# Performance work log

Measured on AMD Instinct MI355X. Metric: run time of the kernel, lower is better.

The kernel has to match this reference:

```python
import jax, jax.numpy as jnp
import numpy as np

B, N_IN, N_OUT, H = 64, 5023, 5023, 256
EPS = 1e-12  # matches torch F.normalize default eps


def setup_inputs() -> dict:
    key = jax.random.key(0)
    k1, k2, k3, k4 = jax.random.split(key, 4)
    return {
        "x": jax.random.normal(k1, (B, N_IN, 3), dtype=jnp.float32),
        "key_w": jax.random.normal(k2, (N_IN, H), dtype=jnp.float32) * (1.0 / np.sqrt(H)),
        "query_w": jax.random.normal(k3, (H, N_OUT), dtype=jnp.float32) * (1.0 / np.sqrt(H)),
        "value_w": jax.random.normal(k4, (3, 3), dtype=jnp.float32),
    }


def reference(x, key_w, query_w, value_w):
    # v = nn.Linear(3,3,bias=False)(x): x @ W^T        [B, N_in, 3]
    v = jnp.einsum("bnd,ed->bne", x, value_w)
    # score = (key @ query) / sqrt(hidden_dim)          [N_in, N_out]
    scale = jnp.asarray(key_w.shape[-1], x.dtype) ** 0.5
    score = jnp.matmul(key_w, query_w) / scale
    # L1 normalization along dim=1 (F.normalize p=1)
    l1 = jnp.sum(jnp.abs(score), axis=1, keepdims=True)
    score = score / jnp.maximum(l1, EPS)
    # y = score.T @ v (dropout is identity in eval / p=0) [B, N_out, 3]
    return jnp.einsum("io,bid->bod", score, v)
```

## Files before the change

kernel.cpp:

```cpp
#include <hip/hip_runtime.h>
#include <hip/hip_bf16.h>

#define N_IN   5023
#define B_SZ   64
#define H_DIM  256
#define NPAD   5120
#define NBD    192
#define SPLITZ 20
#define OUT_ELEMS (B_SZ * N_IN * 3)

typedef short bf16x8 __attribute__((ext_vector_type(8)));
typedef float f32x4  __attribute__((ext_vector_type(4)));

__device__ inline void async_copy16(const void* g, void* l) {
    __builtin_amdgcn_global_load_lds(
        (const __attribute__((address_space(1))) unsigned int*)g,
        (__attribute__((address_space(3))) unsigned int*)l,
        16, 0, 0);
}

__global__ void conv_key_all(const float* __restrict__ kw, short* __restrict__ keyb,
                             short* __restrict__ keyT, float* __restrict__ l1) {
    __shared__ float tile[32][33];
    const int hb = blockIdx.x * 32;
    const int ib = blockIdx.y * 32;
    const int tx = threadIdx.x;
    const int ty = threadIdx.y;
    __hip_bfloat16* kb = (__hip_bfloat16*)keyb;
    __hip_bfloat16* kt = (__hip_bfloat16*)keyT;
    for (int j = 0; j < 32; j += 8) {
        int i = ib + ty + j;
        int h = hb + tx;
        float v = (i < N_IN) ? kw[(size_t)i * H_DIM + h] : 0.0f;
        tile[ty + j][tx] = v;
        kb[(size_t)i * H_DIM + h] = __float2bfloat16(v);
    }
    __syncthreads();
    for (int j = 0; j < 32; j += 8) {
        int h = hb + ty + j;
        int i = ib + tx;
        kt[(size_t)h * NPAD + i] = __float2bfloat16(tile[tx][ty + j]);
    }
    if (blockIdx.x == 0 && ty == 0) l1[ib + tx] = 0.0f;
}

__global__ void conv_qt(const float* __restrict__ qw, short* __restrict__ qtb) {
    __shared__ float tile[32][33];
    const int hb = blockIdx.x * 32;
    const int ob = blockIdx.y * 32;
    const int tx = threadIdx.x;
    const int ty = threadIdx.y;
    for (int j = 0; j < 32; j += 8) {
        int h = hb + ty + j;
        int o = ob + tx;
        tile[ty + j][tx] = (o < N_IN) ? qw[(size_t)h * N_IN + o] * 0.0625f : 0.0f;
    }
    __syncthreads();
    __hip_bfloat16* qt = (__hip_bfloat16*)qtb;
    for (int j = 0; j < 32; j += 8) {
        int o = ob + ty + j;
        int h = hb + tx;
        qt[(size_t)o * H_DIM + h] = __float2bfloat16(tile[tx][ty + j]);
    }
}

__launch_bounds__(256)
__global__ void gemm_l1(const short* __restrict__ qt, const short* __restrict__ keyb,
                        float* __restrict__ l1) {
    __shared__ short As[128 * 64];
    __shared__ short Bs[128 * 64];
    const int bm = blockIdx.x, bn = blockIdx.y;
    const int tid = threadIdx.x, lane = tid & 63, wid = tid >> 6;
    const int wave_m = wid >> 1, wave_n = wid & 1;
    const int srow = lane >> 3;
    const int scol = (lane & 7) * 8;

    f32x4 acc[4][4];
    const f32x4 zf = {0.f, 0.f, 0.f, 0.f};
    for (int a = 0; a < 4; ++a)
        for (int b = 0; b < 4; ++b) acc[a][b] = zf;

    for (int kb = 0; kb < H_DIM; kb += 64) {
        __syncthreads();
        for (int c = 0; c < 4; ++c) {
            int q = wid * 4 + c;
            int row = q * 8 + srow;
            async_copy16(qt   + (size_t)(bm * 128 + row) * H_DIM + kb + scol, As + q * 512);
            async_copy16(keyb + (size_t)(bn * 128 + row) * H_DIM + kb + scol, Bs + q * 512);
        }
        __syncthreads();
        for (int kk = 0; kk < 64; kk += 32) {
            bf16x8 af[4], bf[4];
            int ko = kk + (lane >> 4) * 8;
            for (int t = 0; t < 4; ++t) {
                af[t] = *(const bf16x8*)(As + (wave_m * 64 + t * 16 + (lane & 15)) * 64 + ko);
                bf[t] = *(const bf16x8*)(Bs + (wave_n * 64 + t * 16 + (lane & 15)) * 64 + ko);
            }
            for (int tm = 0; tm < 4; ++tm)
                for (int tn = 0; tn < 4; ++tn)
                    acc[tm][tn] = __builtin_amdgcn_mfma_f32_16x16x32_bf16(
                        af[tm], bf[tn], acc[tm][tn], 0, 0, 0);
        }
    }

    const int quad = lane >> 4, cit = lane & 15;
    for (int tn = 0; tn < 4; ++tn) {
        int ig = bn * 128 + wave_n * 64 + tn * 16 + cit;
        float p = 0.0f;
        for (int tm = 0; tm < 4; ++tm) {
            f32x4 c = acc[tm][tn];
            p += fabsf(c.x) + fabsf(c.y) + fabsf(c.z) + fabsf(c.w);
        }
        p += __shfl_xor(p, 16);
        p += __shfl_xor(p, 32);
        if (quad == 0) atomicAdd(&l1[ig], p);
    }
}

__global__ void build_vmat(const float* __restrict__ x, const float* __restrict__ vw,
                           const float* __restrict__ l1, short* __restrict__ vmatT) {
    int idx = blockIdx.x * 256 + threadIdx.x;
    if (idx >= B_SZ * NPAD) return;
    int b = idx / NPAD, i = idx % NPAD;
    __hip_bfloat16* vt = (__hip_bfloat16*)vmatT;
    if (i < N_IN) {
        const float* xp = x + ((size_t)b * N_IN + i) * 3;
        float x0 = xp[0], x1 = xp[1], x2 = xp[2];
        float r = 1.0f / fmaxf(l1[i], 1e-12f);
        for (int e = 0; e < 3; ++e) {
            float v = x0 * vw[e * 3 + 0] + x1 * vw[e * 3 + 1] + x2 * vw[e * 3 + 2];
            vt[(size_t)(b * 3 + e) * NPAD + i] = __float2bfloat16(v * r);
        }
    } else {
        for (int e = 0; e < 3; ++e)
            vt[(size_t)(b * 3 + e) * NPAD + i] = __float2bfloat16(0.0f);
    }
}

__launch_bounds__(256)
__global__ void gemm3(const short* __restrict__ vmatT, const short* __restrict__ keyT,
                      float* __restrict__ part2) {
    __shared__ short As[192 * 64];
    __shared__ short Bs[64 * 64];
    const int bh = blockIdx.x;
    const int z  = blockIdx.y;
    const int tid = threadIdx.x, lane = tid & 63, wid = tid >> 6;
    const int wave_m = wid >> 1, wave_n = wid & 1;
    const int srow = lane >> 3, scol = (lane & 7) * 8;
    const int quad = lane >> 4, cit = lane & 15;

    f32x4 acc[6][2];
    const f32x4 zf = {0.f, 0.f, 0.f, 0.f};
    for (int a = 0; a < 6; ++a)
        for (int b = 0; b < 2; ++b) acc[a][b] = zf;

    const int kbeg = z * (NPAD / SPLITZ);
    for (int kb = kbeg; kb < kbeg + NPAD / SPLITZ; kb += 64) {
        __syncthreads();
        for (int c = 0; c < 6; ++c) {
            int q = wid * 6 + c;
            int row = q * 8 + srow;
            async_copy16(vmatT + (size_t)row * NPAD + kb + scol, As + q * 512);
        }
        for (int c = 0; c < 2; ++c) {
            int q = wid * 2 + c;
            int row = q * 8 + srow;
            async_copy16(keyT + (size_t)(bh * 64 + row) * NPAD + kb + scol, Bs + q * 512);
        }
        __syncthreads();
        for (int kk = 0; kk < 64; kk += 32) {
            bf16x8 af[6], bf[2];
            int ko = kk + quad * 8;
            for (int t = 0; t < 6; ++t)
                af[t] = *(const bf16x8*)(As + (wave_m * 96 + t * 16 + cit) * 64 + ko);
            for (int t = 0; t < 2; ++t)
                bf[t] = *(const bf16x8*)(Bs + (wave_n * 32 + t * 16 + cit) * 64 + ko);
            for (int tm = 0; tm < 6; ++tm)
                for (int tn = 0; tn < 2; ++tn)
                    acc[tm][tn] = __builtin_amdgcn_mfma_f32_16x16x32_bf16(
                        af[tm], bf[tn], acc[tm][tn], 0, 0, 0);
        }
    }

    float* pz = part2 + (size_t)z * (NBD * H_DIM);
    for (int tn = 0; tn < 2; ++tn) {
        int h = bh * 64 + wave_n * 32 + tn * 16 + cit;
        for (int tm = 0; tm < 6; ++tm) {
            int bd0 = wave_m * 96 + tm * 16 + quad * 4;
            f32x4 c = acc[tm][tn];
            for (int r = 0; r < 4; ++r)
                pz[(size_t)(bd0 + r) * H_DIM + h] = c[r];
        }
    }
}

__global__ void reduce_T(const float* __restrict__ part2, short* __restrict__ T) {
    int idx = blockIdx.x * 256 + threadIdx.x;
    float s = 0.0f;
    for (int z = 0; z < SPLITZ; ++z)
        s += part2[(size_t)z * (NBD * H_DIM) + idx];
    ((__hip_bfloat16*)T)[idx] = __float2bfloat16(s);
}

#define CS_PITCH 196
__launch_bounds__(256)
__global__ void gemm4(const short* __restrict__ qt, const short* __restrict__ T,
                      float* __restrict__ out) {
    __shared__ char smem[64 * CS_PITCH * 4];
    short* As = (short*)smem;
    short* Bs = As + 64 * 64;
    const int bm = blockIdx.x;
    const int tid = threadIdx.x, lane = tid & 63, wid = tid >> 6;
    const int wave_m = wid >> 1, wave_n = wid & 1;
    const int srow = lane >> 3, scol = (lane & 7) * 8;
    const int quad = lane >> 4, cit = lane & 15;

    f32x4 acc[2][6];
    const f32x4 zf = {0.f, 0.f, 0.f, 0.f};
    for (int a = 0; a < 2; ++a)
        for (int b = 0; b < 6; ++b) acc[a][b] = zf;

    for (int kb = 0; kb < H_DIM; kb += 64) {
        __syncthreads();
        for (int c = 0; c < 2; ++c) {
            int q = wid * 2 + c;
            int row = q * 8 + srow;
            async_copy16(qt + (size_t)(bm * 64 + row) * H_DIM + kb + scol, As + q * 512);
        }
        for (int c = 0; c < 6; ++c) {
            int q = wid * 6 + c;
            int row = q * 8 + srow;
            async_copy16(T + (size_t)row * H_DIM + kb + scol, Bs + q * 512);
        }
        __syncthreads();
        for (int kk = 0; kk < 64; kk += 32) {
            bf16x8 af[2], bf[6];
            int ko = kk + quad * 8;
            for (int t = 0; t < 2; ++t)
                af[t] = *(const bf16x8*)(As + (wave_m * 32 + t * 16 + cit) * 64 + ko);
            for (int t = 0; t < 6; ++t)
                bf[t] = *(const bf16x8*)(Bs + (wave_n * 96 + t * 16 + cit) * 64 + ko);
            for (int tm = 0; tm < 2; ++tm)
                for (int tn = 0; tn < 6; ++tn)
                    acc[tm][tn] = __builtin_amdgcn_mfma_f32_16x16x32_bf16(
                        af[tm], bf[tn], acc[tm][tn], 0, 0, 0);
        }
    }

    __syncthreads();
    float* cs = (float*)smem;
    for (int tn = 0; tn < 6; ++tn) {
        int bd = wave_n * 96 + tn * 16 + cit;
        for (int tm = 0; tm < 2; ++tm) {
            int o0 = wave_m * 32 + tm * 16 + quad * 4;
            f32x4 c = acc[tm][tn];
            for (int r = 0; r < 4; ++r)
                cs[(o0 + r) * CS_PITCH + bd] = c[r];
        }
    }
    __syncthreads();
    for (int it = 0; it < 48; ++it) {
        int flat = it * 256 + tid;
        int b = flat / NBD;
        int w = flat - b * NBD;
        int o_l = w / 3, d = w - o_l * 3;
        int og = bm * 64 + o_l;
        if (og < N_IN)
            out[(size_t)b * (N_IN * 3) + (size_t)og * 3 + d] =
                cs[o_l * CS_PITCH + b * 3 + d];
    }
}

extern "C" void kernel_launch(void* const* d_in, const int* in_sizes, int n_in,
                              void* d_out, int out_size, void* d_ws, size_t ws_size,
                              hipStream_t stream) {
    const float* x  = (const float*)d_in[0];
    const float* kw = (const float*)d_in[1];
    const float* qw = (const float*)d_in[2];
    const float* vw = (const float*)d_in[3];
    float* out = (float*)d_out;

    char* w = (char*)d_ws;
    short* keyb  = (short*)(w + 0);
    short* qtb   = (short*)(w + 2621440);
    short* keyT  = (short*)(w + 5242880);
    short* vmatT = (short*)(w + 7864320);
    float* l1    = (float*)(w + 9830400);
    float* part2 = (float*)(w + 9850880);
    short* T     = (short*)(w + 13783040);

    conv_key_all<<<dim3(H_DIM / 32, NPAD / 32), dim3(32, 8), 0, stream>>>(kw, keyb, keyT, l1);
    conv_qt<<<dim3(H_DIM / 32, NPAD / 32), dim3(32, 8), 0, stream>>>(qw, qtb);
    gemm_l1<<<dim3(NPAD / 128, NPAD / 128), 256, 0, stream>>>(qtb, keyb, l1);
    build_vmat<<<(B_SZ * NPAD) / 256, 256, 0, stream>>>(x, vw, l1, vmatT);
    gemm3<<<dim3(H_DIM / 64, SPLITZ), 256, 0, stream>>>(vmatT, keyT, part2);
    reduce_T<<<(NBD * H_DIM) / 256, 256, 0, stream>>>(part2, T);
    gemm4<<<NPAD / 64, 256, 0, stream>>>(qtb, T, out);
}
```

Before: 115.1 us.

## Compute L1 norm GEMM in FP8 with swizzled LDS layout

Adds a conversion kernel that packs the bf16 query and key matrices into FP8, with the query scaled by 16 to keep values in FP8 range. The L1-norm GEMM then uses the fp8 MFMA instruction over 128-wide K chunks with an XOR-swizzled LDS layout, halving the operand bytes and the number of K iterations. build_vmat divides the 16x scale back out. The trade is an extra conversion pass over both matrices and lower precision in the row-sum norms.

```diff
diff --git a/kernel.cpp b/kernel.cpp
--- a/kernel.cpp
+++ b/kernel.cpp
@@ -64,46 +64,67 @@
     }
 }
 
+#define HALF_ELEMS (NPAD * H_DIM / 2)
+__global__ void conv_fp8(const short* __restrict__ qtb, const short* __restrict__ keyb,
+                         unsigned short* __restrict__ q8, unsigned short* __restrict__ k8) {
+    int idx = blockIdx.x * 256 + threadIdx.x;
+    bool isK = idx >= HALF_ELEMS;
+    int p = isK ? idx - HALF_ELEMS : idx;
+    const __hip_bfloat16* src = (const __hip_bfloat16*)(isK ? keyb : qtb);
+    float a = __bfloat162float(src[2 * p]);
+    float b = __bfloat162float(src[2 * p + 1]);
+    if (!isK) { a *= 16.0f; b *= 16.0f; }
+    int packed = __builtin_amdgcn_cvt_pk_fp8_f32(a, b, 0, false);
+    (isK ? k8 : q8)[p] = (unsigned short)(packed & 0xFFFF);
+}
+
 __launch_bounds__(256)
-__global__ void gemm_l1(const short* __restrict__ qt, const short* __restrict__ keyb,
+__global__ void gemm_l1(const unsigned char* __restrict__ q8,
+                        const unsigned char* __restrict__ k8,
                         float* __restrict__ l1) {
-    __shared__ short As[128 * 64];
-    __shared__ short Bs[128 * 64];
+    __shared__ unsigned char As8[128 * 128];
+    __shared__ unsigned char Bs8[128 * 128];
     const int bm = blockIdx.x, bn = blockIdx.y;
     const int tid = threadIdx.x, lane = tid & 63, wid = tid >> 6;
     const int wave_m = wid >> 1, wave_n = wid & 1;
-    const int srow = lane >> 3;
-    const int scol = (lane & 7) * 8;
+    const int r = lane >> 3;
+    const int s = lane & 7;
+    const int quad = lane >> 4, cit = lane & 15;
+    const int xk = cit & 7;
 
     f32x4 acc[4][4];
     const f32x4 zf = {0.f, 0.f, 0.f, 0.f};
     for (int a = 0; a < 4; ++a)
         for (int b = 0; b < 4; ++b) acc[a][b] = zf;
 
-    for (int kb = 0; kb < H_DIM; kb += 64) {
-        __syncthreads();
+    for (int kb = 0; kb < H_DIM; kb += 128) {
+        __syncthreads();
+        const int koff = kb + ((s ^ r) << 4);
         for (int c = 0; c < 4; ++c) {
             int q = wid * 4 + c;
-            int row = q * 8 + srow;
-            async_copy16(qt   + (size_t)(bm * 128 + row) * H_DIM + kb + scol, As + q * 512);
-            async_copy16(keyb + (size_t)(bn * 128 + row) * H_DIM + kb + scol, Bs + q * 512);
-        }
-        __syncthreads();
-        for (int kk = 0; kk < 64; kk += 32) {
-            bf16x8 af[4], bf[4];
-            int ko = kk + (lane >> 4) * 8;
+            int row = q * 8 + r;
+            async_copy16(q8 + (size_t)(bm * 128 + row) * H_DIM + koff, As8 + q * 1024);
+            async_copy16(k8 + (size_t)(bn * 128 + row) * H_DIM + koff, Bs8 + q * 1024);
+        }
+        __syncthreads();
+        for (int ki = 0; ki < 4; ++ki) {
+            int g = ki * 2 + (quad >> 1);
+            int lo8 = (quad & 1) << 3;
+            int slot = ((g ^ xk) << 4) + lo8;
+            long af[4], bf[4];
             for (int t = 0; t < 4; ++t) {
-                af[t] = *(const bf16x8*)(As + (wave_m * 64 + t * 16 + (lane & 15)) * 64 + ko);
-                bf[t] = *(const bf16x8*)(Bs + (wave_n * 64 + t * 16 + (lane & 15)) * 64 + ko);
+                int am = wave_m * 64 + t * 16 + cit;
+                af[t] = *(const long*)(As8 + am * 128 + slot);
+                int bn_ = wave_n * 64 + t * 16 + cit;
+                bf[t] = *(const long*)(Bs8 + bn_ * 128 + slot);
             }
             for (int tm = 0; tm < 4; ++tm)
                 for (int tn = 0; tn < 4; ++tn)
-                    acc[tm][tn] = __builtin_amdgcn_mfma_f32_16x16x32_bf16(
+                    acc[tm][tn] = __builtin_amdgcn_mfma_f32_16x16x32_fp8_fp8(
                         af[tm], bf[tn], acc[tm][tn], 0, 0, 0);
         }
     }
 
-    const int quad = lane >> 4, cit = lane & 15;
     for (int tn = 0; tn < 4; ++tn) {
         int ig = bn * 128 + wave_n * 64 + tn * 16 + cit;
         float p = 0.0f;
@@ -126,7 +147,7 @@
     if (i < N_IN) {
         const float* xp = x + ((size_t)b * N_IN + i) * 3;
         float x0 = xp[0], x1 = xp[1], x2 = xp[2];
-        float r = 1.0f / fmaxf(l1[i], 1e-12f);
+        float r = 1.0f / fmaxf(l1[i] * 0.0625f, 1e-12f);
         for (int e = 0; e < 3; ++e) {
             float v = x0 * vw[e * 3 + 0] + x1 * vw[e * 3 + 1] + x2 * vw[e * 3 + 2];
             vt[(size_t)(b * 3 + e) * NPAD + i] = __float2bfloat16(v * r);
@@ -288,10 +309,14 @@
     float* l1    = (float*)(w + 9830400);
     float* part2 = (float*)(w + 9850880);
     short* T     = (short*)(w + 13783040);
+    unsigned short* q8 = (unsigned short*)(w + 13881344);
+    unsigned short* k8 = (unsigned short*)(w + 15192064);
 
     conv_key_all<<<dim3(H_DIM / 32, NPAD / 32), dim3(32, 8), 0, stream>>>(kw, keyb, keyT, l1);
     conv_qt<<<dim3(H_DIM / 32, NPAD / 32), dim3(32, 8), 0, stream>>>(qw, qtb);
-    gemm_l1<<<dim3(NPAD / 128, NPAD / 128), 256, 0, stream>>>(qtb, keyb, l1);
+    conv_fp8<<<(2 * HALF_ELEMS) / 256, 256, 0, stream>>>(qtb, keyb, q8, k8);
+    gemm_l1<<<dim3(NPAD / 128, NPAD / 128), 256, 0, stream>>>(
+        (const unsigned char*)q8, (const unsigned char*)k8, l1);
     build_vmat<<<(B_SZ * NPAD) / 256, 256, 0, stream>>>(x, vw, l1, vmatT);
     gemm3<<<dim3(H_DIM / 64, SPLITZ), 256, 0, stream>>>(vmatT, keyT, part2);
     reduce_T<<<(NBD * H_DIM) / 256, 256, 0, stream>>>(part2, T);
```

Result: faster. 111.6 us (-3.1%).
